# Kernel tuning notes

Hardware: AMD Instinct MI355X
Metric: run time of the kernel (lower is better)

Reference implementation:

```python
import jax, jax.numpy as jnp
import numpy as np

B, TQ, TK, H = 8, 64, 8192, 256


def setup_inputs() -> dict:
    key = jax.random.key(0)
    k1, k2, k3, k4 = jax.random.split(key, 4)
    query = jax.random.normal(k1, (B, TQ, H), dtype=jnp.float32)
    keys = jax.random.normal(k2, (B, TK, H), dtype=jnp.float32)
    # nn.Linear(H, H): weight [H, H], bias [H]; scale like torch default-ish
    Wa_w = jax.random.normal(k3, (H, H), dtype=jnp.float32) * (1.0 / np.sqrt(H))
    Wa_b = jax.random.normal(k4, (H,), dtype=jnp.float32) * 0.01
    return {"query": query, "keys": keys, "Wa_w": Wa_w, "Wa_b": Wa_b}


def reference(query, keys, Wa_w, Wa_b):
    # keys_transformed = keys @ Wa_w.T + Wa_b  (torch Linear semantics)
    keys_t = jnp.einsum('bkh,oh->bko', keys, Wa_w) + Wa_b  # [B,TK,H]
    scores = jnp.einsum('bqh,bkh->bqk', query, keys_t)       # [B,TQ,TK]
    weights = jax.nn.softmax(scores, axis=-1)
    context = jnp.einsum('bqk,bkh->bqh', weights, keys)      # [B,TQ,H]
    return (context, weights)
```

## Files before the change

kernel.cpp:

```cpp
#include <hip/hip_runtime.h>

#define B 8
#define TQ 64
#define TK 8192
#define H 256

#define KSPLIT 32
#define KPB (TK / KSPLIT)
#define CRS 72

typedef __attribute__((ext_vector_type(8))) short bf16x8;
typedef __attribute__((ext_vector_type(4))) float f32x4;
typedef __attribute__((ext_vector_type(4))) unsigned short u16x4;
typedef __attribute__((ext_vector_type(2))) unsigned int u32x2;

static __device__ inline unsigned short f2bf_rne(float x) {
    unsigned int u = __float_as_uint(x);
    unsigned int r = (u + 0x7fffu + ((u >> 16) & 1u)) >> 16;
    return (unsigned short)r;
}

__global__ __launch_bounds__(256) void qtransform_kernel(
    const float* __restrict__ query, const float* __restrict__ Wa_w,
    const float* __restrict__ Wa_b, unsigned short* __restrict__ qthi,
    unsigned short* __restrict__ qtlo, float* __restrict__ qb)
{
    __shared__ float q_s[H];
    __shared__ float red[4];
    const int r = blockIdx.x;
    const int t = threadIdx.x;
    q_s[t] = query[r * H + t];
    __syncthreads();

    float a0 = 0.f, a1 = 0.f, a2 = 0.f, a3 = 0.f;
    for (int o = 0; o < H; o += 4) {
        a0 += q_s[o + 0] * Wa_w[(o + 0) * H + t];
        a1 += q_s[o + 1] * Wa_w[(o + 1) * H + t];
        a2 += q_s[o + 2] * Wa_w[(o + 2) * H + t];
        a3 += q_s[o + 3] * Wa_w[(o + 3) * H + t];
    }
    const float s = (a0 + a1) + (a2 + a3);
    const unsigned int u = __float_as_uint(s);
    const float hif = __uint_as_float(u & 0xFFFF0000u);
    const float lof = s - hif;
    qthi[r * H + t] = (unsigned short)(u >> 16);
    qtlo[r * H + t] = (unsigned short)(__float_as_uint(lof) >> 16);

    float p = q_s[t] * Wa_b[t];
    for (int off = 32; off > 0; off >>= 1) p += __shfl_down(p, off, 64);
    if ((t & 63) == 0) red[t >> 6] = p;
    __syncthreads();
    if (t == 0) qb[r] = (red[0] + red[1]) + (red[2] + red[3]);
}


#define STAGE1(v, row, khb) {                                                  \
    unsigned int u0=__float_as_uint(v.x), u1=__float_as_uint(v.y);             \
    unsigned int u2=__float_as_uint(v.z), u3=__float_as_uint(v.w);             \
    unsigned int h01=(u0>>16)|(u1&0xFFFF0000u), h23=(u2>>16)|(u3&0xFFFF0000u); \
    float l0=v.x-__uint_as_float(u0&0xFFFF0000u);                              \
    float l1=v.y-__uint_as_float(u1&0xFFFF0000u);                              \
    float l2=v.z-__uint_as_float(u2&0xFFFF0000u);                              \
    float l3=v.w-__uint_as_float(u3&0xFFFF0000u);                              \
    unsigned int q01=(__float_as_uint(l0)>>16)|(__float_as_uint(l1)&0xFFFF0000u); \
    unsigned int q23=(__float_as_uint(l2)>>16)|(__float_as_uint(l3)&0xFFFF0000u); \
    int bo=(row)*128 + (((hf>>1)^((row)&7))<<4) + ((hf&1)<<3);                 \
    *(u32x2*)((char*)b_hi+bo) = (u32x2){h01,h23};                              \
    *(u32x2*)((char*)b_lo+bo) = (u32x2){q01,q23};                              \
    *(u32x2*)&khb[(size_t)(row)*H + hf*4] = (u32x2){h01,h23}; }

#define LOADCHUNK(d0,d1,d2,d3, hc)                                             \
    d0 = *(const float4*)&kbase_g[(size_t)(sr +  0) * H + (hc) + hf * 4];      \
    d1 = *(const float4*)&kbase_g[(size_t)(sr + 16) * H + (hc) + hf * 4];      \
    d2 = *(const float4*)&kbase_g[(size_t)(sr + 32) * H + (hc) + hf * 4];      \
    d3 = *(const float4*)&kbase_g[(size_t)(sr + 48) * H + (hc) + hf * 4];

#define STAGECHUNK(v0,v1,v2,v3, hc) {                                          \
    unsigned short* khb = khi_ws + ((size_t)b * TK + k0g) * H + (hc);          \
    STAGE1(v0, sr +  0, khb); STAGE1(v1, sr + 16, khb);                        \
    STAGE1(v2, sr + 32, khb); STAGE1(v3, sr + 48, khb); }

#define COMPUTE(hc) {                                                          \
    _Pragma("unroll")                                                          \
    for (int hs = 0; hs < 64; hs += 32) {                                      \
        bf16x8 ah = *(const bf16x8*)&ah_base[(hc) + hs + lgrp * 8];            \
        bf16x8 al = *(const bf16x8*)&al_base[(hc) + hs + lgrp * 8];            \
        _Pragma("unroll")                                                      \
        for (int nt = 0; nt < 4; ++nt) {                                       \
            int rr = 16 * nt + lrow;                                           \
            int rb = rr * 128 + ((((hs >> 3) + lgrp) ^ (rr & 7)) << 4);        \
            bf16x8 bh = *(const bf16x8*)((const char*)b_hi + rb);              \
            bf16x8 bl = *(const bf16x8*)((const char*)b_lo + rb);              \
            acc[nt] = __builtin_amdgcn_mfma_f32_16x16x32_bf16(ah, bh, acc[nt], 0, 0, 0); \
            acc[nt] = __builtin_amdgcn_mfma_f32_16x16x32_bf16(ah, bl, acc[nt], 0, 0, 0); \
            acc[nt] = __builtin_amdgcn_mfma_f32_16x16x32_bf16(al, bh, acc[nt], 0, 0, 0); \
        } } }

__global__ __launch_bounds__(256, 4) void scores_kernel(
    const unsigned short* __restrict__ qthi, const unsigned short* __restrict__ qtlo,
    const float* __restrict__ qb, const float* __restrict__ keys,
    unsigned short* __restrict__ khi_ws, float* __restrict__ wout)
{
    __shared__ unsigned short b_hi[64 * 64];
    __shared__ unsigned short b_lo[64 * 64];
    const int t    = threadIdx.x;
    const int kt   = blockIdx.x;
    const int b    = blockIdx.y;
    const int k0g  = kt * 64;
    const int w    = t >> 6;
    const int lane = t & 63;
    const int lrow = lane & 15;
    const int lgrp = lane >> 4;
    const int sr   = t >> 4;
    const int hf   = t & 15;

    const float* kbase_g = keys + (size_t)(b * TK + k0g) * H;
    const unsigned short* ah_base = qthi + (size_t)(b * TQ + 16 * w + lrow) * H;
    const unsigned short* al_base = qtlo + (size_t)(b * TQ + 16 * w + lrow) * H;

    f32x4 acc[4];
    #pragma unroll
    for (int nt = 0; nt < 4; ++nt) acc[nt] = (f32x4){0.f, 0.f, 0.f, 0.f};

    float4 r0, r1, r2, r3, p0, p1, p2, p3;
    LOADCHUNK(r0, r1, r2, r3, 0)

    LOADCHUNK(p0, p1, p2, p3, 64)
    STAGECHUNK(r0, r1, r2, r3, 0)
    __syncthreads();
    COMPUTE(0)
    __syncthreads();

    LOADCHUNK(r0, r1, r2, r3, 128)
    STAGECHUNK(p0, p1, p2, p3, 64)
    __syncthreads();
    COMPUTE(64)
    __syncthreads();

    LOADCHUNK(p0, p1, p2, p3, 192)
    STAGECHUNK(r0, r1, r2, r3, 128)
    __syncthreads();
    COMPUTE(128)
    __syncthreads();

    STAGECHUNK(p0, p1, p2, p3, 192)
    __syncthreads();
    COMPUTE(192)

    #pragma unroll
    for (int j = 0; j < 4; ++j) {
        const int qrow = 16 * w + lgrp * 4 + j;
        const float bias = qb[b * TQ + qrow];
        float* dst = &wout[(size_t)(b * TQ + qrow) * TK + k0g + lrow];
        #pragma unroll
        for (int nt = 0; nt < 4; ++nt) dst[16 * nt] = acc[nt][j] + bias;
    }
}

__global__ __launch_bounds__(1024) void softmax_kernel(
    float* __restrict__ w, unsigned short* __restrict__ phi)
{
    const int r = blockIdx.x;
    const int t = threadIdx.x;
    float4* row4 = (float4*)(w + (size_t)r * TK);
    __shared__ float redm[16];
    __shared__ float reds[16];
    const int wid = t >> 6, lane = t & 63;

    float4 v0 = row4[t];
    float4 v1 = row4[t + 1024];
    float m = fmaxf(fmaxf(fmaxf(v0.x, v0.y), fmaxf(v0.z, v0.w)),
                    fmaxf(fmaxf(v1.x, v1.y), fmaxf(v1.z, v1.w)));
    for (int off = 32; off > 0; off >>= 1) m = fmaxf(m, __shfl_xor(m, off, 64));
    if (lane == 0) redm[wid] = m;
    __syncthreads();
    m = redm[0];
    #pragma unroll
    for (int i = 1; i < 16; ++i) m = fmaxf(m, redm[i]);

    v0.x = __expf(v0.x - m); v0.y = __expf(v0.y - m);
    v0.z = __expf(v0.z - m); v0.w = __expf(v0.w - m);
    v1.x = __expf(v1.x - m); v1.y = __expf(v1.y - m);
    v1.z = __expf(v1.z - m); v1.w = __expf(v1.w - m);
    float s = (v0.x + v0.y + v0.z + v0.w) + (v1.x + v1.y + v1.z + v1.w);
    for (int off = 32; off > 0; off >>= 1) s += __shfl_xor(s, off, 64);
    if (lane == 0) reds[wid] = s;
    __syncthreads();
    s = reds[0];
    #pragma unroll
    for (int i = 1; i < 16; ++i) s += reds[i];
    const float inv = 1.0f / s;

    v0.x *= inv; v0.y *= inv; v0.z *= inv; v0.w *= inv;
    v1.x *= inv; v1.y *= inv; v1.z *= inv; v1.w *= inv;
    row4[t] = v0;
    row4[t + 1024] = v1;

    unsigned short* prow = phi + (size_t)r * TK;
    u16x4 pk0, pk1;
    pk0[0] = f2bf_rne(v0.x); pk0[1] = f2bf_rne(v0.y);
    pk0[2] = f2bf_rne(v0.z); pk0[3] = f2bf_rne(v0.w);
    pk1[0] = f2bf_rne(v1.x); pk1[1] = f2bf_rne(v1.y);
    pk1[2] = f2bf_rne(v1.z); pk1[3] = f2bf_rne(v1.w);
    *(u16x4*)&prow[t * 4] = pk0;
    *(u16x4*)&prow[4096 + t * 4] = pk1;
}

__global__ __launch_bounds__(256) void context_main_kernel(
    const unsigned short* __restrict__ phi, const unsigned short* __restrict__ khi,
    float* __restrict__ part)
{
    __shared__ unsigned short kT[64 * CRS];
    const int t    = threadIdx.x;
    const int ks   = blockIdx.x;
    const int ht   = blockIdx.y;
    const int b    = blockIdx.z;
    const int w    = t >> 6;
    const int lane = t & 63;
    const int lrow = lane & 15;
    const int lgrp = lane >> 4;

    f32x4 acc[4];
    #pragma unroll
    for (int nt = 0; nt < 4; ++nt) acc[nt] = (f32x4){0.f, 0.f, 0.f, 0.f};

    const int kbase = ks * KPB;
    for (int c = 0; c < KPB; c += 64) {
        __syncthreads();
        #pragma unroll
        for (int i = 0; i < 4; ++i) {
            int idx = t + 256 * i;
            int k = idx >> 4, hq = idx & 15;
            u16x4 v = *(const u16x4*)&khi[((size_t)b * TK + kbase + c + k) * H + ht * 64 + hq * 4];
            #pragma unroll
            for (int c4 = 0; c4 < 4; ++c4) {
                int h = hq * 4 + c4;
                kT[h * CRS + (((k >> 3) ^ ((h >> 3) & 7)) << 3) + (k & 7)] = v[c4];
            }
        }
        __syncthreads();
        #pragma unroll
        for (int kc = 0; kc < 64; kc += 32) {
            bf16x8 af = *(const bf16x8*)&phi[((size_t)(b * TQ) + 16 * w + lrow) * TK
                                             + kbase + c + kc + lgrp * 8];
            #pragma unroll
            for (int nt = 0; nt < 4; ++nt) {
                int h = 16 * nt + lrow;
                bf16x8 bfg = *(const bf16x8*)&kT[h * CRS
                              + ((((kc >> 3) + lgrp) ^ ((h >> 3) & 7)) << 3)];
                acc[nt] = __builtin_amdgcn_mfma_f32_16x16x32_bf16(af, bfg, acc[nt], 0, 0, 0);
            }
        }
    }
    float* dst = part + (size_t)ks * (B * TQ * H);
    #pragma unroll
    for (int j = 0; j < 4; ++j) {
        const int qrow = 16 * w + lgrp * 4 + j;
        #pragma unroll
        for (int nt = 0; nt < 4; ++nt)
            dst[(size_t)(b * TQ + qrow) * H + ht * 64 + 16 * nt + lrow] = acc[nt][j];
    }
}

__global__ __launch_bounds__(256) void context_reduce_kernel(
    const float* __restrict__ part, float* __restrict__ ctx)
{
    const int idx = blockIdx.x * 256 + threadIdx.x;
    float4 s = make_float4(0.f, 0.f, 0.f, 0.f);
    #pragma unroll 8
    for (int ks = 0; ks < KSPLIT; ++ks) {
        float4 v = *(const float4*)&part[(size_t)ks * (B * TQ * H) + (size_t)idx * 4];
        s.x += v.x; s.y += v.y; s.z += v.z; s.w += v.w;
    }
    *(float4*)&ctx[(size_t)idx * 4] = s;
}

extern "C" void kernel_launch(void* const* d_in, const int* in_sizes, int n_in,
                              void* d_out, int out_size, void* d_ws, size_t ws_size,
                              hipStream_t stream) {
    const float* query = (const float*)d_in[0];
    const float* keys  = (const float*)d_in[1];
    const float* Wa_w  = (const float*)d_in[2];
    const float* Wa_b  = (const float*)d_in[3];

    float* ctx = (float*)d_out;
    float* wts = (float*)d_out + B * TQ * H;

    char* p = (char*)d_ws;
    float* part = (float*)p;                    p += (size_t)KSPLIT * B * TQ * H * 4;
    unsigned short* khi = (unsigned short*)p;   p += (size_t)B * TK * H * 2;
    unsigned short* phi = (unsigned short*)p;   p += (size_t)B * TQ * TK * 2;
    unsigned short* qthi = (unsigned short*)p;  p += (size_t)B * TQ * H * 2;
    unsigned short* qtlo = (unsigned short*)p;  p += (size_t)B * TQ * H * 2;
    float* qb = (float*)p;

    qtransform_kernel<<<B * TQ, 256, 0, stream>>>(query, Wa_w, Wa_b, qthi, qtlo, qb);
    scores_kernel<<<dim3(TK / 64, B), 256, 0, stream>>>(qthi, qtlo, qb, keys, khi, wts);
    softmax_kernel<<<B * TQ, 1024, 0, stream>>>(wts, phi);
    context_main_kernel<<<dim3(KSPLIT, 4, B), 256, 0, stream>>>(phi, khi, part);
    context_reduce_kernel<<<(B * TQ * H / 4) / 256, 256, 0, stream>>>(part, ctx);
}
```

Before: 146.6 us.

## Load keys directly into MFMA registers and drop bf16 key workspace

The scores kernel no longer stages key tiles through shared memory. Each wave now loads its own 16 key rows straight from global memory into MFMA B-operand registers, splits them into hi/lo bf16 in registers, and loops over all four query m-tiles, so the LDS buffers and barriers go away. The context kernel now reads fp32 keys and truncates them to bf16 itself instead of reading a bf16 copy written by the scores kernel, which removes the workspace write. The cost is that the context kernel reads twice as many key bytes, and the scores kernel now issues strided per-lane global loads and repeated query-operand loads from global or cache.

New measurement: 167.8 us. 1.14x slower.

```diff
diff --git a/kernel.cpp b/kernel.cpp
--- a/kernel.cpp
+++ b/kernel.cpp
@@ -12,7 +12,9 @@
 typedef __attribute__((ext_vector_type(8))) short bf16x8;
 typedef __attribute__((ext_vector_type(4))) float f32x4;
 typedef __attribute__((ext_vector_type(4))) unsigned short u16x4;
-typedef __attribute__((ext_vector_type(2))) unsigned int u32x2;
+typedef __attribute__((ext_vector_type(4))) unsigned int u32x4;
+
+union bfcast { u32x4 u; bf16x8 b; };
 
 static __device__ inline unsigned short f2bf_rne(float x) {
     unsigned int u = __float_as_uint(x);
@@ -53,56 +55,11 @@
     if (t == 0) qb[r] = (red[0] + red[1]) + (red[2] + red[3]);
 }
 
-
-#define STAGE1(v, row, khb) {                                                  \
-    unsigned int u0=__float_as_uint(v.x), u1=__float_as_uint(v.y);             \
-    unsigned int u2=__float_as_uint(v.z), u3=__float_as_uint(v.w);             \
-    unsigned int h01=(u0>>16)|(u1&0xFFFF0000u), h23=(u2>>16)|(u3&0xFFFF0000u); \
-    float l0=v.x-__uint_as_float(u0&0xFFFF0000u);                              \
-    float l1=v.y-__uint_as_float(u1&0xFFFF0000u);                              \
-    float l2=v.z-__uint_as_float(u2&0xFFFF0000u);                              \
-    float l3=v.w-__uint_as_float(u3&0xFFFF0000u);                              \
-    unsigned int q01=(__float_as_uint(l0)>>16)|(__float_as_uint(l1)&0xFFFF0000u); \
-    unsigned int q23=(__float_as_uint(l2)>>16)|(__float_as_uint(l3)&0xFFFF0000u); \
-    int bo=(row)*128 + (((hf>>1)^((row)&7))<<4) + ((hf&1)<<3);                 \
-    *(u32x2*)((char*)b_hi+bo) = (u32x2){h01,h23};                              \
-    *(u32x2*)((char*)b_lo+bo) = (u32x2){q01,q23};                              \
-    *(u32x2*)&khb[(size_t)(row)*H + hf*4] = (u32x2){h01,h23}; }
-
-#define LOADCHUNK(d0,d1,d2,d3, hc)                                             \
-    d0 = *(const float4*)&kbase_g[(size_t)(sr +  0) * H + (hc) + hf * 4];      \
-    d1 = *(const float4*)&kbase_g[(size_t)(sr + 16) * H + (hc) + hf * 4];      \
-    d2 = *(const float4*)&kbase_g[(size_t)(sr + 32) * H + (hc) + hf * 4];      \
-    d3 = *(const float4*)&kbase_g[(size_t)(sr + 48) * H + (hc) + hf * 4];
-
-#define STAGECHUNK(v0,v1,v2,v3, hc) {                                          \
-    unsigned short* khb = khi_ws + ((size_t)b * TK + k0g) * H + (hc);          \
-    STAGE1(v0, sr +  0, khb); STAGE1(v1, sr + 16, khb);                        \
-    STAGE1(v2, sr + 32, khb); STAGE1(v3, sr + 48, khb); }
-
-#define COMPUTE(hc) {                                                          \
-    _Pragma("unroll")                                                          \
-    for (int hs = 0; hs < 64; hs += 32) {                                      \
-        bf16x8 ah = *(const bf16x8*)&ah_base[(hc) + hs + lgrp * 8];            \
-        bf16x8 al = *(const bf16x8*)&al_base[(hc) + hs + lgrp * 8];            \
-        _Pragma("unroll")                                                      \
-        for (int nt = 0; nt < 4; ++nt) {                                       \
-            int rr = 16 * nt + lrow;                                           \
-            int rb = rr * 128 + ((((hs >> 3) + lgrp) ^ (rr & 7)) << 4);        \
-            bf16x8 bh = *(const bf16x8*)((const char*)b_hi + rb);              \
-            bf16x8 bl = *(const bf16x8*)((const char*)b_lo + rb);              \
-            acc[nt] = __builtin_amdgcn_mfma_f32_16x16x32_bf16(ah, bh, acc[nt], 0, 0, 0); \
-            acc[nt] = __builtin_amdgcn_mfma_f32_16x16x32_bf16(ah, bl, acc[nt], 0, 0, 0); \
-            acc[nt] = __builtin_amdgcn_mfma_f32_16x16x32_bf16(al, bh, acc[nt], 0, 0, 0); \
-        } } }
-
 __global__ __launch_bounds__(256, 4) void scores_kernel(
     const unsigned short* __restrict__ qthi, const unsigned short* __restrict__ qtlo,
     const float* __restrict__ qb, const float* __restrict__ keys,
-    unsigned short* __restrict__ khi_ws, float* __restrict__ wout)
-{
-    __shared__ unsigned short b_hi[64 * 64];
-    __shared__ unsigned short b_lo[64 * 64];
+    float* __restrict__ wout)
+{
     const int t    = threadIdx.x;
     const int kt   = blockIdx.x;
     const int b    = blockIdx.y;
@@ -111,50 +68,55 @@
     const int lane = t & 63;
     const int lrow = lane & 15;
     const int lgrp = lane >> 4;
-    const int sr   = t >> 4;
-    const int hf   = t & 15;
-
-    const float* kbase_g = keys + (size_t)(b * TK + k0g) * H;
-    const unsigned short* ah_base = qthi + (size_t)(b * TQ + 16 * w + lrow) * H;
-    const unsigned short* al_base = qtlo + (size_t)(b * TQ + 16 * w + lrow) * H;
+
+    const float* krow = keys + (size_t)(b * TK + k0g + 16 * w + lrow) * H + lgrp * 8;
+    const unsigned short* ahb = qthi + (size_t)(b * TQ + lrow) * H + lgrp * 8;
+    const unsigned short* alb = qtlo + (size_t)(b * TQ + lrow) * H + lgrp * 8;
 
     f32x4 acc[4];
     #pragma unroll
-    for (int nt = 0; nt < 4; ++nt) acc[nt] = (f32x4){0.f, 0.f, 0.f, 0.f};
-
-    float4 r0, r1, r2, r3, p0, p1, p2, p3;
-    LOADCHUNK(r0, r1, r2, r3, 0)
-
-    LOADCHUNK(p0, p1, p2, p3, 64)
-    STAGECHUNK(r0, r1, r2, r3, 0)
-    __syncthreads();
-    COMPUTE(0)
-    __syncthreads();
-
-    LOADCHUNK(r0, r1, r2, r3, 128)
-    STAGECHUNK(p0, p1, p2, p3, 64)
-    __syncthreads();
-    COMPUTE(64)
-    __syncthreads();
-
-    LOADCHUNK(p0, p1, p2, p3, 192)
-    STAGECHUNK(r0, r1, r2, r3, 128)
-    __syncthreads();
-    COMPUTE(128)
-    __syncthreads();
-
-    STAGECHUNK(p0, p1, p2, p3, 192)
-    __syncthreads();
-    COMPUTE(192)
-
-    #pragma unroll
-    for (int j = 0; j < 4; ++j) {
-        const int qrow = 16 * w + lgrp * 4 + j;
-        const float bias = qb[b * TQ + qrow];
-        float* dst = &wout[(size_t)(b * TQ + qrow) * TK + k0g + lrow];
-        #pragma unroll
-        for (int nt = 0; nt < 4; ++nt) dst[16 * nt] = acc[nt][j] + bias;
-    }
+    for (int mt = 0; mt < 4; ++mt) acc[mt] = (f32x4){0.f, 0.f, 0.f, 0.f};
+
+    #pragma unroll 4
+    for (int hs = 0; hs < H; hs += 32) {
+        float4 kv0 = *(const float4*)&krow[hs];
+        float4 kv1 = *(const float4*)&krow[hs + 4];
+        unsigned int u0 = __float_as_uint(kv0.x), u1 = __float_as_uint(kv0.y);
+        unsigned int u2 = __float_as_uint(kv0.z), u3 = __float_as_uint(kv0.w);
+        unsigned int u4 = __float_as_uint(kv1.x), u5 = __float_as_uint(kv1.y);
+        unsigned int u6 = __float_as_uint(kv1.z), u7 = __float_as_uint(kv1.w);
+        bfcast bh, bl;
+        bh.u = (u32x4){(u0 >> 16) | (u1 & 0xFFFF0000u), (u2 >> 16) | (u3 & 0xFFFF0000u),
+                       (u4 >> 16) | (u5 & 0xFFFF0000u), (u6 >> 16) | (u7 & 0xFFFF0000u)};
+        float l0 = kv0.x - __uint_as_float(u0 & 0xFFFF0000u);
+        float l1 = kv0.y - __uint_as_float(u1 & 0xFFFF0000u);
+        float l2 = kv0.z - __uint_as_float(u2 & 0xFFFF0000u);
+        float l3 = kv0.w - __uint_as_float(u3 & 0xFFFF0000u);
+        float l4 = kv1.x - __uint_as_float(u4 & 0xFFFF0000u);
+        float l5 = kv1.y - __uint_as_float(u5 & 0xFFFF0000u);
+        float l6 = kv1.z - __uint_as_float(u6 & 0xFFFF0000u);
+        float l7 = kv1.w - __uint_as_float(u7 & 0xFFFF0000u);
+        bl.u = (u32x4){(__float_as_uint(l0) >> 16) | (__float_as_uint(l1) & 0xFFFF0000u),
+                       (__float_as_uint(l2) >> 16) | (__float_as_uint(l3) & 0xFFFF0000u),
+                       (__float_as_uint(l4) >> 16) | (__float_as_uint(l5) & 0xFFFF0000u),
+                       (__float_as_uint(l6) >> 16) | (__float_as_uint(l7) & 0xFFFF0000u)};
+        #pragma unroll
+        for (int mt = 0; mt < 4; ++mt) {
+            bf16x8 ah = *(const bf16x8*)&ahb[(size_t)(16 * mt) * H + hs];
+            bf16x8 al = *(const bf16x8*)&alb[(size_t)(16 * mt) * H + hs];
+            acc[mt] = __builtin_amdgcn_mfma_f32_16x16x32_bf16(ah, bh.b, acc[mt], 0, 0, 0);
+            acc[mt] = __builtin_amdgcn_mfma_f32_16x16x32_bf16(ah, bl.b, acc[mt], 0, 0, 0);
+            acc[mt] = __builtin_amdgcn_mfma_f32_16x16x32_bf16(al, bh.b, acc[mt], 0, 0, 0);
+        }
+    }
+    const int kcol = k0g + 16 * w + lrow;
+    #pragma unroll
+    for (int mt = 0; mt < 4; ++mt)
+        #pragma unroll
+        for (int j = 0; j < 4; ++j) {
+            const int qrow = 16 * mt + lgrp * 4 + j;
+            wout[(size_t)(b * TQ + qrow) * TK + kcol] = acc[mt][j] + qb[b * TQ + qrow];
+        }
 }
 
 __global__ __launch_bounds__(1024) void softmax_kernel(
@@ -207,7 +169,7 @@
 }
 
 __global__ __launch_bounds__(256) void context_main_kernel(
-    const unsigned short* __restrict__ phi, const unsigned short* __restrict__ khi,
+    const unsigned short* __restrict__ phi, const float* __restrict__ keys,
     float* __restrict__ part)
 {
     __shared__ unsigned short kT[64 * CRS];
@@ -231,11 +193,16 @@
         for (int i = 0; i < 4; ++i) {
             int idx = t + 256 * i;
             int k = idx >> 4, hq = idx & 15;
-            u16x4 v = *(const u16x4*)&khi[((size_t)b * TK + kbase + c + k) * H + ht * 64 + hq * 4];
+            float4 v = *(const float4*)&keys[((size_t)b * TK + kbase + c + k) * H + ht * 64 + hq * 4];
+            unsigned short e[4];
+            e[0] = (unsigned short)(__float_as_uint(v.x) >> 16);
+            e[1] = (unsigned short)(__float_as_uint(v.y) >> 16);
+            e[2] = (unsigned short)(__float_as_uint(v.z) >> 16);
+            e[3] = (unsigned short)(__float_as_uint(v.w) >> 16);
             #pragma unroll
             for (int c4 = 0; c4 < 4; ++c4) {
                 int h = hq * 4 + c4;
-                kT[h * CRS + (((k >> 3) ^ ((h >> 3) & 7)) << 3) + (k & 7)] = v[c4];
+                kT[h * CRS + (((k >> 3) ^ ((h >> 3) & 7)) << 3) + (k & 7)] = e[c4];
             }
         }
         __syncthreads();
@@ -288,15 +255,14 @@
 
     char* p = (char*)d_ws;
     float* part = (float*)p;                    p += (size_t)KSPLIT * B * TQ * H * 4;
-    unsigned short* khi = (unsigned short*)p;   p += (size_t)B * TK * H * 2;
     unsigned short* phi = (unsigned short*)p;   p += (size_t)B * TQ * TK * 2;
     unsigned short* qthi = (unsigned short*)p;  p += (size_t)B * TQ * H * 2;
     unsigned short* qtlo = (unsigned short*)p;  p += (size_t)B * TQ * H * 2;
     float* qb = (float*)p;
 
     qtransform_kernel<<<B * TQ, 256, 0, stream>>>(query, Wa_w, Wa_b, qthi, qtlo, qb);
-    scores_kernel<<<dim3(TK / 64, B), 256, 0, stream>>>(qthi, qtlo, qb, keys, khi, wts);
+    scores_kernel<<<dim3(TK / 64, B), 256, 0, stream>>>(qthi, qtlo, qb, keys, wts);
     softmax_kernel<<<B * TQ, 1024, 0, stream>>>(wts, phi);
-    context_main_kernel<<<dim3(KSPLIT, 4, B), 256, 0, stream>>>(phi, khi, part);
+    context_main_kernel<<<dim3(KSPLIT, 4, B), 256, 0, stream>>>(phi, keys, part);
     context_reduce_kernel<<<(B * TQ * H / 4) / 256, 256, 0, stream>>>(part, ctx);
 }
```

## Fuse softmax into scores and context kernels via per-tile partial max/sum

Applied to the files above, without the earlier changes.

The scores kernel now writes raw scores plus a per-64-key-tile max and sum-of-exponentials for each query row. A small row-reduce kernel combines these into the row max and inverse sum, and the context kernel recomputes the normalized probabilities from raw scores on the fly. That kernel also writes the fp32 weights output (from the ht==0 blocks) and feeds bf16 probabilities into the MFMA. This removes the separate softmax pass, its full read-modify-write of the weight matrix, and the bf16 probability buffer. In exchange, the context kernel reads fp32 scores instead of bf16 probabilities, and the four ht blocks each redo the exp.

After: 152.9 us. 1.04x slower.

```diff
diff --git a/kernel.cpp b/kernel.cpp
--- a/kernel.cpp
+++ b/kernel.cpp
@@ -99,7 +99,8 @@
 __global__ __launch_bounds__(256, 4) void scores_kernel(
     const unsigned short* __restrict__ qthi, const unsigned short* __restrict__ qtlo,
     const float* __restrict__ qb, const float* __restrict__ keys,
-    unsigned short* __restrict__ khi_ws, float* __restrict__ wout)
+    unsigned short* __restrict__ khi_ws, float* __restrict__ sraw,
+    float* __restrict__ pm, float* __restrict__ ps)
 {
     __shared__ unsigned short b_hi[64 * 64];
     __shared__ unsigned short b_lo[64 * 64];
@@ -151,64 +152,50 @@
     for (int j = 0; j < 4; ++j) {
         const int qrow = 16 * w + lgrp * 4 + j;
         const float bias = qb[b * TQ + qrow];
-        float* dst = &wout[(size_t)(b * TQ + qrow) * TK + k0g + lrow];
-        #pragma unroll
-        for (int nt = 0; nt < 4; ++nt) dst[16 * nt] = acc[nt][j] + bias;
-    }
-}
-
-__global__ __launch_bounds__(1024) void softmax_kernel(
-    float* __restrict__ w, unsigned short* __restrict__ phi)
+        float v0 = acc[0][j] + bias, v1 = acc[1][j] + bias;
+        float v2 = acc[2][j] + bias, v3 = acc[3][j] + bias;
+        float* dst = &sraw[(size_t)(b * TQ + qrow) * TK + k0g + lrow];
+        dst[0] = v0; dst[16] = v1; dst[32] = v2; dst[48] = v3;
+        float m = fmaxf(fmaxf(v0, v1), fmaxf(v2, v3));
+        m = fmaxf(m, __shfl_xor(m, 1, 64));
+        m = fmaxf(m, __shfl_xor(m, 2, 64));
+        m = fmaxf(m, __shfl_xor(m, 4, 64));
+        m = fmaxf(m, __shfl_xor(m, 8, 64));
+        float e = __expf(v0 - m) + __expf(v1 - m) + __expf(v2 - m) + __expf(v3 - m);
+        e += __shfl_xor(e, 1, 64);
+        e += __shfl_xor(e, 2, 64);
+        e += __shfl_xor(e, 4, 64);
+        e += __shfl_xor(e, 8, 64);
+        if (lrow == 0) {
+            pm[(size_t)(b * TQ + qrow) * 128 + kt] = m;
+            ps[(size_t)(b * TQ + qrow) * 128 + kt] = e;
+        }
+    }
+}
+
+__global__ __launch_bounds__(128) void rowreduce_kernel(
+    const float* __restrict__ pm, const float* __restrict__ ps,
+    float* __restrict__ Mrow, float* __restrict__ Sinv)
 {
     const int r = blockIdx.x;
     const int t = threadIdx.x;
-    float4* row4 = (float4*)(w + (size_t)r * TK);
-    __shared__ float redm[16];
-    __shared__ float reds[16];
-    const int wid = t >> 6, lane = t & 63;
-
-    float4 v0 = row4[t];
-    float4 v1 = row4[t + 1024];
-    float m = fmaxf(fmaxf(fmaxf(v0.x, v0.y), fmaxf(v0.z, v0.w)),
-                    fmaxf(fmaxf(v1.x, v1.y), fmaxf(v1.z, v1.w)));
+    __shared__ float mred[2], sred[2];
+    float m = pm[(size_t)r * 128 + t];
     for (int off = 32; off > 0; off >>= 1) m = fmaxf(m, __shfl_xor(m, off, 64));
-    if (lane == 0) redm[wid] = m;
-    __syncthreads();
-    m = redm[0];
-    #pragma unroll
-    for (int i = 1; i < 16; ++i) m = fmaxf(m, redm[i]);
-
-    v0.x = __expf(v0.x - m); v0.y = __expf(v0.y - m);
-    v0.z = __expf(v0.z - m); v0.w = __expf(v0.w - m);
-    v1.x = __expf(v1.x - m); v1.y = __expf(v1.y - m);
-    v1.z = __expf(v1.z - m); v1.w = __expf(v1.w - m);
-    float s = (v0.x + v0.y + v0.z + v0.w) + (v1.x + v1.y + v1.z + v1.w);
+    if ((t & 63) == 0) mred[t >> 6] = m;
+    __syncthreads();
+    const float M = fmaxf(mred[0], mred[1]);
+    float s = ps[(size_t)r * 128 + t] * __expf(pm[(size_t)r * 128 + t] - M);
     for (int off = 32; off > 0; off >>= 1) s += __shfl_xor(s, off, 64);
-    if (lane == 0) reds[wid] = s;
-    __syncthreads();
-    s = reds[0];
-    #pragma unroll
-    for (int i = 1; i < 16; ++i) s += reds[i];
-    const float inv = 1.0f / s;
-
-    v0.x *= inv; v0.y *= inv; v0.z *= inv; v0.w *= inv;
-    v1.x *= inv; v1.y *= inv; v1.z *= inv; v1.w *= inv;
-    row4[t] = v0;
-    row4[t + 1024] = v1;
-
-    unsigned short* prow = phi + (size_t)r * TK;
-    u16x4 pk0, pk1;
-    pk0[0] = f2bf_rne(v0.x); pk0[1] = f2bf_rne(v0.y);
-    pk0[2] = f2bf_rne(v0.z); pk0[3] = f2bf_rne(v0.w);
-    pk1[0] = f2bf_rne(v1.x); pk1[1] = f2bf_rne(v1.y);
-    pk1[2] = f2bf_rne(v1.z); pk1[3] = f2bf_rne(v1.w);
-    *(u16x4*)&prow[t * 4] = pk0;
-    *(u16x4*)&prow[4096 + t * 4] = pk1;
+    if ((t & 63) == 0) sred[t >> 6] = s;
+    __syncthreads();
+    if (t == 0) { Mrow[r] = M; Sinv[r] = 1.0f / (sred[0] + sred[1]); }
 }
 
 __global__ __launch_bounds__(256) void context_main_kernel(
-    const unsigned short* __restrict__ phi, const unsigned short* __restrict__ khi,
-    float* __restrict__ part)
+    const float* __restrict__ sraw, const float* __restrict__ Mrow,
+    const float* __restrict__ Sinv, const unsigned short* __restrict__ khi,
+    float* __restrict__ part, float* __restrict__ wts)
 {
     __shared__ unsigned short kT[64 * CRS];
     const int t    = threadIdx.x;
@@ -219,6 +206,10 @@
     const int lane = t & 63;
     const int lrow = lane & 15;
     const int lgrp = lane >> 4;
+
+    const int qrow = b * TQ + 16 * w + lrow;
+    const float M  = Mrow[qrow];
+    const float Si = Sinv[qrow];
 
     f32x4 acc[4];
     #pragma unroll
@@ -241,24 +232,40 @@
         __syncthreads();
         #pragma unroll
         for (int kc = 0; kc < 64; kc += 32) {
-            bf16x8 af = *(const bf16x8*)&phi[((size_t)(b * TQ) + 16 * w + lrow) * TK
-                                             + kbase + c + kc + lgrp * 8];
+            const size_t koff = (size_t)qrow * TK + kbase + c + kc + lgrp * 8;
+            float4 s0 = *(const float4*)&sraw[koff];
+            float4 s1 = *(const float4*)&sraw[koff + 4];
+            float p0 = __expf(s0.x - M) * Si, p1 = __expf(s0.y - M) * Si;
+            float p2 = __expf(s0.z - M) * Si, p3 = __expf(s0.w - M) * Si;
+            float p4 = __expf(s1.x - M) * Si, p5 = __expf(s1.y - M) * Si;
+            float p6 = __expf(s1.z - M) * Si, p7 = __expf(s1.w - M) * Si;
+            if (ht == 0) {
+                *(float4*)&wts[koff] = make_float4(p0, p1, p2, p3);
+                *(float4*)&wts[koff + 4] = make_float4(p4, p5, p6, p7);
+            }
+            u16x4 af0, af1;
+            af0[0] = f2bf_rne(p0); af0[1] = f2bf_rne(p1);
+            af0[2] = f2bf_rne(p2); af0[3] = f2bf_rne(p3);
+            af1[0] = f2bf_rne(p4); af1[1] = f2bf_rne(p5);
+            af1[2] = f2bf_rne(p6); af1[3] = f2bf_rne(p7);
+            union { u16x4 u[2]; bf16x8 b; } afu;
+            afu.u[0] = af0; afu.u[1] = af1;
             #pragma unroll
             for (int nt = 0; nt < 4; ++nt) {
                 int h = 16 * nt + lrow;
                 bf16x8 bfg = *(const bf16x8*)&kT[h * CRS
                               + ((((kc >> 3) + lgrp) ^ ((h >> 3) & 7)) << 3)];
-                acc[nt] = __builtin_amdgcn_mfma_f32_16x16x32_bf16(af, bfg, acc[nt], 0, 0, 0);
+                acc[nt] = __builtin_amdgcn_mfma_f32_16x16x32_bf16(afu.b, bfg, acc[nt], 0, 0, 0);
             }
         }
     }
     float* dst = part + (size_t)ks * (B * TQ * H);
     #pragma unroll
     for (int j = 0; j < 4; ++j) {
-        const int qrow = 16 * w + lgrp * 4 + j;
+        const int qr = 16 * w + lgrp * 4 + j;
         #pragma unroll
         for (int nt = 0; nt < 4; ++nt)
-            dst[(size_t)(b * TQ + qrow) * H + ht * 64 + 16 * nt + lrow] = acc[nt][j];
+            dst[(size_t)(b * TQ + qr) * H + ht * 64 + 16 * nt + lrow] = acc[nt][j];
     }
 }
 
@@ -289,14 +296,18 @@
     char* p = (char*)d_ws;
     float* part = (float*)p;                    p += (size_t)KSPLIT * B * TQ * H * 4;
     unsigned short* khi = (unsigned short*)p;   p += (size_t)B * TK * H * 2;
-    unsigned short* phi = (unsigned short*)p;   p += (size_t)B * TQ * TK * 2;
+    float* sraw = (float*)p;                    p += (size_t)B * TQ * TK * 4;
+    float* pm = (float*)p;                      p += (size_t)B * TQ * 128 * 4;
+    float* ps = (float*)p;                      p += (size_t)B * TQ * 128 * 4;
+    float* Mr = (float*)p;                      p += (size_t)B * TQ * 4;
+    float* Sv = (float*)p;                      p += (size_t)B * TQ * 4;
     unsigned short* qthi = (unsigned short*)p;  p += (size_t)B * TQ * H * 2;
     unsigned short* qtlo = (unsigned short*)p;  p += (size_t)B * TQ * H * 2;
     float* qb = (float*)p;
 
     qtransform_kernel<<<B * TQ, 256, 0, stream>>>(query, Wa_w, Wa_b, qthi, qtlo, qb);
-    scores_kernel<<<dim3(TK / 64, B), 256, 0, stream>>>(qthi, qtlo, qb, keys, khi, wts);
-    softmax_kernel<<<B * TQ, 1024, 0, stream>>>(wts, phi);
-    context_main_kernel<<<dim3(KSPLIT, 4, B), 256, 0, stream>>>(phi, khi, part);
+    scores_kernel<<<dim3(TK / 64, B), 256, 0, stream>>>(qthi, qtlo, qb, keys, khi, sraw, pm, ps);
+    rowreduce_kernel<<<B * TQ, 128, 0, stream>>>(pm, ps, Mr, Sv);
+    context_main_kernel<<<dim3(KSPLIT, 4, B), 256, 0, stream>>>(sraw, Mr, Sv, khi, part, wts);
     context_reduce_kernel<<<(B * TQ * H / 4) / 256, 256, 0, stream>>>(part, ctx);
 }
```
